# Optimization experiments

Measured on AMD Instinct MI355X. Metric: run time of the kernel, lower is better.

## Reference

```python
import math
import jax, jax.numpy as jnp
import numpy as np

# ---- model dims ----
D = 4096          # hidden_size
N = 32            # num_attention_heads (== num_key_value_heads)
Q_LORA = 1536
KV_LORA = 512
QK_NOPE = 128
QK_ROPE = 64
QK_HEAD = QK_NOPE + QK_ROPE   # 192
V_HEAD = 128
EPS = 1e-6
T = 2048

# ---- yarn rope constants ----
ROPE_THETA = 10000.0
FACTOR = 40.0
ORIG_MAX = 4096
BETA_FAST = 32.0
BETA_SLOW = 1.0
MSCALE = 1.0
MSCALE_ALL_DIM = 1.0


def _yarn_get_mscale(scale, mscale):
    if scale <= 1.0:
        return 1.0
    return 0.1 * mscale * math.log(scale) + 1.0

# softmax scale: qk_head_dim^-0.5 * yarn_mscale^2 (rope_mscale_all_dim = 1.0)
YARN_MSCALE = _yarn_get_mscale(FACTOR, MSCALE_ALL_DIM)
SM_SCALE = QK_HEAD ** (-0.5) * YARN_MSCALE ** 2


def _yarn_cos_sin(positions):
    """DeepSeek yarn scaled rotary embeddings. positions: int [T]."""
    half = QK_ROPE // 2
    pow_ = np.arange(0, QK_ROPE, 2, dtype=np.float64) / QK_ROPE
    pos_freqs = ROPE_THETA ** pow_
    inv_extra = 1.0 / pos_freqs
    inv_inter = 1.0 / (FACTOR * pos_freqs)

    def corr_dim(n_rot):
        return (QK_ROPE * math.log(ORIG_MAX / (n_rot * 2 * math.pi))) / (2 * math.log(ROPE_THETA))

    low = max(math.floor(corr_dim(BETA_FAST)), 0)
    high = min(math.ceil(corr_dim(BETA_SLOW)), QK_ROPE - 1)
    ramp = np.clip((np.arange(half, dtype=np.float64) - low) / max(high - low, 1e-3), 0.0, 1.0)
    mask = 1.0 - ramp  # 1 where extrapolation
    inv_freq = inv_inter * (1.0 - mask) + inv_extra * mask
    inv_freq = jnp.asarray(inv_freq, jnp.float32)

    mscale_coef = _yarn_get_mscale(FACTOR, MSCALE) / _yarn_get_mscale(FACTOR, MSCALE_ALL_DIM)
    t = positions.astype(jnp.float32)
    freqs = t[:, None] * inv_freq[None, :]          # [T, half]
    return jnp.cos(freqs) * mscale_coef, jnp.sin(freqs) * mscale_coef


def _apply_rope(x_tnh, cos, sin):
    """Neox-style (split halves) rope. x: [T, N, QK_ROPE]; cos/sin: [T, half]."""
    half = QK_ROPE // 2
    x1, x2 = x_tnh[..., :half], x_tnh[..., half:]
    c, s = cos[:, None, :], sin[:, None, :]
    return jnp.concatenate([x1 * c - x2 * s, x1 * s + x2 * c], axis=-1)


def _rms_norm(x, scale, eps=EPS):
    var = jnp.mean(jnp.square(x), axis=-1, keepdims=True)
    return x * jax.lax.rsqrt(var + eps) * scale


def setup_inputs() -> dict:
    key = jax.random.key(0)
    ks = jax.random.split(key, 8)
    std = 0.02
    return {
        "x": jax.random.normal(ks[0], (T, D), jnp.float32),
        "positions": jnp.arange(T, dtype=jnp.int32),
        "w_q_down": jax.random.normal(ks[1], (D, Q_LORA), jnp.float32) * std,
        "q_norm_scale": jnp.ones((Q_LORA,), jnp.float32),
        "w_q_up": jax.random.normal(ks[2], (Q_LORA, N, QK_HEAD), jnp.float32) * std,
        "w_kv_down": jax.random.normal(ks[3], (D, KV_LORA + QK_ROPE), jnp.float32) * std,
        "kv_norm_scale": jnp.ones((KV_LORA,), jnp.float32),
        "w_kv_up": jax.random.normal(ks[4], (KV_LORA, N, QK_NOPE + V_HEAD), jnp.float32) * std,
        "w_o": jax.random.normal(ks[5], (N, V_HEAD, D), jnp.float32) * std,
    }


def reference(x, positions, w_q_down, q_norm_scale, w_q_up, w_kv_down,
              kv_norm_scale, w_kv_up, w_o):
    cos, sin = _yarn_cos_sin(positions)

    # ---- q projection (low rank) ----
    q_ta = _rms_norm(jnp.einsum('td,da->ta', x, w_q_down), q_norm_scale)
    q_tnh = jnp.einsum('ta,anh->tnh', q_ta, w_q_up)            # [T,N,192]
    q_rope = _apply_rope(q_tnh[..., QK_NOPE:], cos, sin)
    q_tnh = jnp.concatenate([q_tnh[..., :QK_NOPE], q_rope], axis=-1)

    # ---- kv projection (compressed latent) ----
    kv_sa = jnp.einsum('sd,da->sa', x, w_kv_down)              # [T, KV_LORA+64]
    k_rope = _apply_rope(kv_sa[:, None, KV_LORA:], cos, sin)   # [T,1,64]
    k_rope = jnp.broadcast_to(k_rope, (x.shape[0], N, QK_ROPE))
    kv_lat = _rms_norm(kv_sa[..., :KV_LORA], kv_norm_scale)
    kv_nope = jnp.einsum('sa,anh->snh', kv_lat, w_kv_up)       # [T,N,256]
    k_snh = jnp.concatenate([kv_nope[..., :QK_NOPE], k_rope], axis=-1)
    v_snh = kv_nope[..., QK_NOPE:]

    # ---- causal attention (prefill; padding to 128-multiple is a no-op) ----
    scores = jnp.einsum('tnh,snh->nts', q_tnh, k_snh) * SM_SCALE
    tpos = jnp.arange(x.shape[0])
    causal = tpos[:, None] >= tpos[None, :]
    scores = jnp.where(causal[None, :, :], scores, jnp.finfo(scores.dtype).min)
    probs = jax.nn.softmax(scores, axis=-1)
    out_tnh = jnp.einsum('nts,snh->tnh', probs, v_snh)

    # ---- output projection ----
    return jnp.einsum('tnh,nhd->td', out_tnh, w_o)
```

## Files before the change

### kernel.cpp

```cpp
#include <hip/hip_runtime.h>
#include <math.h>
#include <stdint.h>

#define T_    2048
#define D_    4096
#define NH_   32
#define QL_   1536
#define KVL_  512
#define ROPE_ 64
#define NOPE_ 128
#define HQK_  192
#define HV_   128
#define KVD_  576
#define NCAT_ 2112

typedef __bf16 bf16x8 __attribute__((ext_vector_type(8)));
typedef __bf16 bf16x4 __attribute__((ext_vector_type(4)));
typedef float f32x4 __attribute__((ext_vector_type(4)));

__device__ __forceinline__ void gload_lds16(const __bf16* g, __bf16* l) {
  __builtin_amdgcn_global_load_lds(
      (const __attribute__((address_space(1))) void*)g,
      (__attribute__((address_space(3))) void*)l, 16, 0, 0);
}

template <typename OutT>
__global__ __launch_bounds__(256, 3) void mfma_gemm_kernel(
    const __bf16* __restrict__ A, const __bf16* __restrict__ Bt,
    OutT* __restrict__ C, int M, int Ncols, int K) {
  __shared__ __bf16 As[128 * 64];
  __shared__ __bf16 Bs[128 * 64];
  const int tid = threadIdx.x;
  const int lane = tid & 63;
  const int w = tid >> 6;
  const int wm = w >> 1, wn = w & 1;
  const int lg = lane >> 4, lj = lane & 15;
  const int bm = blockIdx.y * 128;
  const int bn = blockIdx.x * 128;

  const __bf16* ga[4]; const __bf16* gb[4];
  int ldsoff[4];
  #pragma unroll
  for (int i = 0; i < 4; ++i) {
    int task = i * 256 + tid;
    int r = task >> 3, cl = task & 7;
    int cg = cl ^ (r & 7);
    ga[i] = A  + (size_t)(bm + r) * K + cg * 8;
    gb[i] = Bt + (size_t)(bn + r) * K + cg * 8;
    ldsoff[i] = (i * 256 + w * 64) * 8;
  }

  f32x4 acc[4][4];
  #pragma unroll
  for (int mi = 0; mi < 4; ++mi)
    #pragma unroll
    for (int ni = 0; ni < 4; ++ni) acc[mi][ni] = (f32x4){0.f, 0.f, 0.f, 0.f};

  for (int k0 = 0; k0 < K; k0 += 64) {
    __syncthreads();
    #pragma unroll
    for (int i = 0; i < 4; ++i) gload_lds16(ga[i] + k0, &As[ldsoff[i]]);
    #pragma unroll
    for (int i = 0; i < 4; ++i) gload_lds16(gb[i] + k0, &Bs[ldsoff[i]]);
    __syncthreads();
    #pragma unroll
    for (int kh = 0; kh < 2; ++kh) {
      bf16x8 af[4], bfr[4];
      #pragma unroll
      for (int i = 0; i < 4; ++i) {
        int ra = wm * 64 + i * 16 + lj;
        af[i] = *(const bf16x8*)&As[ra * 64 + ((((kh << 2) + lg) ^ (ra & 7)) << 3)];
      }
      #pragma unroll
      for (int i = 0; i < 4; ++i) {
        int rb = wn * 64 + i * 16 + lj;
        bfr[i] = *(const bf16x8*)&Bs[rb * 64 + ((((kh << 2) + lg) ^ (rb & 7)) << 3)];
      }
      #pragma unroll
      for (int mi = 0; mi < 4; ++mi)
        #pragma unroll
        for (int ni = 0; ni < 4; ++ni)
          acc[mi][ni] = __builtin_amdgcn_mfma_f32_16x16x32_bf16(af[mi], bfr[ni], acc[mi][ni], 0, 0, 0);
    }
  }

  #pragma unroll
  for (int mi = 0; mi < 4; ++mi) {
    #pragma unroll
    for (int r = 0; r < 4; ++r) {
      int row = bm + wm * 64 + mi * 16 + lg * 4 + r;
      #pragma unroll
      for (int ni = 0; ni < 4; ++ni) {
        int col = bn + wn * 64 + ni * 16 + lj;
        if (col < Ncols) C[(size_t)row * Ncols + col] = (OutT)acc[mi][ni][r];
      }
    }
  }
}

__global__ __launch_bounds__(256) void transpose_bf16_kernel(
    const float* __restrict__ B, __bf16* __restrict__ Bt, int K, int N) {
  __shared__ float tile[64][65];
  int n0 = blockIdx.x * 64, k0 = blockIdx.y * 64;
  int tid = threadIdx.x;
  int kr = tid >> 4, nc = (tid & 15) * 4;
  #pragma unroll
  for (int i = 0; i < 4; ++i) {
    int k = kr + i * 16;
    float4 v = make_float4(0.f, 0.f, 0.f, 0.f);
    if (n0 + nc < N) v = *(const float4*)(B + (size_t)(k0 + k) * N + n0 + nc);
    tile[k][nc + 0] = v.x; tile[k][nc + 1] = v.y;
    tile[k][nc + 2] = v.z; tile[k][nc + 3] = v.w;
  }
  __syncthreads();
  int nl = tid >> 4, k4 = (tid & 15) * 4;
  #pragma unroll
  for (int i = 0; i < 4; ++i) {
    int nn = nl + i * 16;
    bf16x4 o;
    o[0] = (__bf16)tile[k4 + 0][nn]; o[1] = (__bf16)tile[k4 + 1][nn];
    o[2] = (__bf16)tile[k4 + 2][nn]; o[3] = (__bf16)tile[k4 + 3][nn];
    *(bf16x4*)(Bt + (size_t)(n0 + nn) * K + k0 + k4) = o;
  }
}

__global__ __launch_bounds__(256) void conv_bf16_kernel(
    const float* __restrict__ in, __bf16* __restrict__ out, int n8) {
  int i = blockIdx.x * 256 + threadIdx.x;
  if (i >= n8) return;
  float4 a = *(const float4*)(in + (size_t)i * 8);
  float4 b = *(const float4*)(in + (size_t)i * 8 + 4);
  bf16x8 v;
  v[0] = (__bf16)a.x; v[1] = (__bf16)a.y; v[2] = (__bf16)a.z; v[3] = (__bf16)a.w;
  v[4] = (__bf16)b.x; v[5] = (__bf16)b.y; v[6] = (__bf16)b.z; v[7] = (__bf16)b.w;
  *(bf16x8*)(out + (size_t)i * 8) = v;
}

__global__ __launch_bounds__(256) void rmsnorm_bf16_kernel(
    const float* __restrict__ in, __bf16* __restrict__ out,
    const float* __restrict__ scale, int len, int in_stride) {
  int row = blockIdx.x;
  const float* x = in + (size_t)row * in_stride;
  __bf16* y = out + (size_t)row * len;
  float ss = 0.f;
  for (int i = threadIdx.x; i < len; i += 256) { float v = x[i]; ss += v * v; }
  __shared__ float red[4];
  #pragma unroll
  for (int o = 32; o > 0; o >>= 1) ss += __shfl_down(ss, o, 64);
  int wid = threadIdx.x >> 6, lane = threadIdx.x & 63;
  if (lane == 0) red[wid] = ss;
  __syncthreads();
  if (threadIdx.x == 0) {
    float t = red[0] + red[1] + red[2] + red[3];
    red[0] = 1.0f / sqrtf(t / (float)len + 1e-6f);
  }
  __syncthreads();
  float r = red[0];
  for (int i = threadIdx.x; i < len; i += 256) y[i] = (__bf16)(x[i] * r * scale[i]);
}

struct InvFreq { float f[32]; };
__global__ __launch_bounds__(256) void rope_table_kernel(
    const int* __restrict__ pos, float* __restrict__ cosT, float* __restrict__ sinT,
    InvFreq invf) {
  int idx = blockIdx.x * 256 + threadIdx.x;
  if (idx >= T_ * 32) return;
  int t = idx >> 5, i = idx & 31;
  float fr = (float)pos[t] * invf.f[i];
  cosT[idx] = cosf(fr);
  sinT[idx] = sinf(fr);
}

__global__ __launch_bounds__(256) void rope_q_kernel(
    __bf16* __restrict__ q, const float* __restrict__ cosT, const float* __restrict__ sinT) {
  int idx = blockIdx.x * 256 + threadIdx.x;
  if (idx >= T_ * NH_ * 32) return;
  int i = idx & 31;
  int tn = idx >> 5;
  int t = tn >> 5;
  __bf16* b = q + (size_t)tn * HQK_ + NOPE_;
  float x1 = (float)b[i], x2 = (float)b[i + 32];
  float c = cosT[t * 32 + i], s = sinT[t * 32 + i];
  b[i]      = (__bf16)(x1 * c - x2 * s);
  b[i + 32] = (__bf16)(x1 * s + x2 * c);
}

__global__ __launch_bounds__(256) void rope_k_kernel(
    const float* __restrict__ src, int stride, const float* __restrict__ cosT,
    const float* __restrict__ sinT, __bf16* __restrict__ k_rope) {
  int idx = blockIdx.x * 256 + threadIdx.x;
  if (idx >= T_ * 32) return;
  int t = idx >> 5, i = idx & 31;
  const float* b = src + (size_t)t * stride;
  float x1 = b[i], x2 = b[i + 32];
  float c = cosT[idx], s = sinT[idx];
  k_rope[t * 64 + i]      = (__bf16)(x1 * c - x2 * s);
  k_rope[t * 64 + i + 32] = (__bf16)(x1 * s + x2 * c);
}

__global__ __launch_bounds__(256) void prep_vt_kernel(
    const __bf16* __restrict__ kv_nopeb, __bf16* __restrict__ Vt) {
  __shared__ __bf16 tile[64][136];
  int s0 = blockIdx.x * 64;
  int n = blockIdx.y;
  int tid = threadIdx.x;
  #pragma unroll
  for (int i = 0; i < 4; ++i) {
    int idx = tid + i * 256;
    int s = idx >> 4, c = idx & 15;
    bf16x8 v = *(const bf16x8*)(kv_nopeb + ((size_t)(s0 + s) * NH_ + n) * 256 + NOPE_ + c * 8);
    *(bf16x8*)&tile[s][c * 8] = v;
  }
  __syncthreads();
  #pragma unroll
  for (int i = 0; i < 8; ++i) {
    int idx = tid + i * 256;
    int h = idx >> 4, s4 = (idx & 15) * 4;
    bf16x4 v;
    v[0] = tile[s4 + 0][h]; v[1] = tile[s4 + 1][h];
    v[2] = tile[s4 + 2][h]; v[3] = tile[s4 + 3][h];
    *(bf16x4*)(Vt + ((size_t)n * HV_ + h) * T_ + s0 + s4) = v;
  }
}

__global__ __launch_bounds__(256) void attn_mfma_kernel(
    const __bf16* __restrict__ q_tnh, const __bf16* __restrict__ kv_nopeb,
    const __bf16* __restrict__ k_rope, const __bf16* __restrict__ Vt,
    __bf16* __restrict__ attn_out, float sm_scale2) {
  __shared__ __bf16 KsL[2][24 * 64 * 8];
  __shared__ __bf16 Vs[8 * 128 * 8];
  __shared__ __bf16 Ps[4][16 * 64];
  const int tid = threadIdx.x;
  const int lane = tid & 63;
  const int w = tid >> 6;
  const int id = blockIdx.x;
  const int j = id >> 3;
  const int qt = 31 - (j >> 2);
  const int n = (id & 7) * 4 + (j & 3);
  const int t0 = qt * 64;
  const int lg = lane >> 4;
  const int lj = lane & 15;
  const int rowbase = t0 + w * 16;

  const __bf16* kptr[6]; size_t kstep[6]; int klds[6];
  #pragma unroll
  for (int i = 0; i < 6; ++i) {
    int task = i * 256 + tid;
    int c = task >> 6, s = task & 63;
    if (c < 16) { kptr[i] = kv_nopeb + ((size_t)s * NH_ + n) * 256 + c * 8; kstep[i] = (size_t)64 * NH_ * 256; }
    else        { kptr[i] = k_rope + (size_t)s * ROPE_ + (c - 16) * 8;      kstep[i] = (size_t)64 * ROPE_; }
    klds[i] = (i * 256 + w * 64) * 8;
  }
  const __bf16* vptr[4]; int vlds[4];
  #pragma unroll
  for (int i = 0; i < 4; ++i) {
    int task = i * 256 + tid;
    int c = task >> 7, h = task & 127;
    vptr[i] = Vt + ((size_t)n * HV_ + h) * T_ + c * 8;
    vlds[i] = (i * 256 + w * 64) * 8;
  }

  #define STAGE_K(bufIdx)                                                      \
    do {                                                                       \
      __bf16* kb_ = &KsL[bufIdx][0];                                           \
      _Pragma("unroll")                                                        \
      for (int i_ = 0; i_ < 6; ++i_) {                                         \
        gload_lds16(kptr[i_], kb_ + klds[i_]);                                 \
        kptr[i_] += kstep[i_];                                                 \
      }                                                                        \
    } while (0)
  #define STAGE_V()                                                            \
    do {                                                                       \
      _Pragma("unroll")                                                        \
      for (int i_ = 0; i_ < 4; ++i_) {                                         \
        gload_lds16(vptr[i_], &Vs[0] + vlds[i_]);                              \
        vptr[i_] += 64;                                                        \
      }                                                                        \
    } while (0)

  STAGE_K(0);

  bf16x8 qf[6];
  {
    int t = t0 + w * 16 + lj;
    const __bf16* qp = q_tnh + ((size_t)t * NH_ + n) * HQK_;
    #pragma unroll
    for (int kk = 0; kk < 6; ++kk) {
      bf16x8 raw = *(const bf16x8*)(qp + kk * 32 + lg * 8);
      bf16x8 v;
      #pragma unroll
      for (int i = 0; i < 8; ++i) v[i] = (__bf16)((float)raw[i] * sm_scale2);
      qf[kk] = v;
    }
  }

  f32x4 O[8];
  #pragma unroll
  for (int nb = 0; nb < 8; ++nb) O[nb] = (f32x4){0.f, 0.f, 0.f, 0.f};
  float m_r[4], l_r[4];
  #pragma unroll
  for (int r = 0; r < 4; ++r) { m_r[r] = -1e30f; l_r[r] = 0.f; }

  __syncthreads();

  const int nst = qt + 1;
  #pragma unroll 1
  for (int st = 0; st < nst; ++st) {
    const int s0 = st * 64;
    const int cur = st & 1;
    if (st + 1 < nst) STAGE_K(cur ^ 1);
    STAGE_V();
    const __bf16* kb = &KsL[cur][0];

    f32x4 S[4];
    __builtin_amdgcn_s_setprio(1);
    #pragma unroll
    for (int sb = 0; sb < 4; ++sb) {
      f32x4 acc = (f32x4){0.f, 0.f, 0.f, 0.f};
      int srow = sb * 16 + lj;
      #pragma unroll
      for (int kk = 0; kk < 6; ++kk) {
        int c = kk * 4 + lg;
        bf16x8 b = *(const bf16x8*)&kb[(c * 64 + srow) * 8];
        acc = __builtin_amdgcn_mfma_f32_16x16x32_bf16(qf[kk], b, acc, 0, 0, 0);
      }
      S[sb] = acc;
    }
    __builtin_amdgcn_s_setprio(0);
    if (st == qt) {
      #pragma unroll
      for (int sb = 0; sb < 4; ++sb)
        #pragma unroll
        for (int r = 0; r < 4; ++r) {
          int row = rowbase + lg * 4 + r;
          int col = s0 + sb * 16 + lj;
          if (col > row) S[sb][r] = -1e30f;
        }
    }
    float mx[4];
    #pragma unroll
    for (int r = 0; r < 4; ++r) {
      float m2 = fmaxf(fmaxf(S[0][r], S[1][r]), fmaxf(S[2][r], S[3][r]));
      m2 = fmaxf(m2, __shfl_xor(m2, 1));
      m2 = fmaxf(m2, __shfl_xor(m2, 2));
      m2 = fmaxf(m2, __shfl_xor(m2, 4));
      m2 = fmaxf(m2, __shfl_xor(m2, 8));
      mx[r] = m2;
    }
    int need = (mx[0] > m_r[0]) | (mx[1] > m_r[1]) | (mx[2] > m_r[2]) | (mx[3] > m_r[3]);
    if (__any(need)) {
      #pragma unroll
      for (int r = 0; r < 4; ++r) {
        float mnew = fmaxf(m_r[r], mx[r]);
        float corr = __builtin_amdgcn_exp2f(m_r[r] - mnew);
        m_r[r] = mnew;
        l_r[r] *= corr;
        #pragma unroll
        for (int nb = 0; nb < 8; ++nb) O[nb][r] = O[nb][r] * corr;
      }
    }
    #pragma unroll
    for (int r = 0; r < 4; ++r) {
      float psum = 0.f;
      #pragma unroll
      for (int sb = 0; sb < 4; ++sb) {
        float pp = __builtin_amdgcn_exp2f(S[sb][r] - m_r[r]);
        S[sb][r] = pp;
        psum += pp;
      }
      l_r[r] += psum;
    }
    #pragma unroll
    for (int sb = 0; sb < 4; ++sb) {
      int sl = sb * 16 + lj;
      int c = sl >> 3;
      #pragma unroll
      for (int r = 0; r < 4; ++r) {
        int rw = lg * 4 + r;
        Ps[w][rw * 64 + ((c ^ (rw & 7)) << 3) + (sl & 7)] = (__bf16)S[sb][r];
      }
    }
    __syncthreads();
    __builtin_amdgcn_s_setprio(1);
    #pragma unroll
    for (int kk = 0; kk < 2; ++kk) {
      int ca = kk * 4 + lg;
      bf16x8 pa = *(const bf16x8*)&Ps[w][lj * 64 + ((ca ^ (lj & 7)) << 3)];
      #pragma unroll
      for (int nb = 0; nb < 8; ++nb) {
        int h = nb * 16 + lj;
        bf16x8 bv = *(const bf16x8*)&Vs[(ca * 128 + h) * 8];
        O[nb] = __builtin_amdgcn_mfma_f32_16x16x32_bf16(pa, bv, O[nb], 0, 0, 0);
      }
    }
    __builtin_amdgcn_s_setprio(0);
    __syncthreads();
  }

  #pragma unroll
  for (int r = 0; r < 4; ++r) {
    float lsum = l_r[r];
    lsum += __shfl_xor(lsum, 1);
    lsum += __shfl_xor(lsum, 2);
    lsum += __shfl_xor(lsum, 4);
    lsum += __shfl_xor(lsum, 8);
    float inv = 1.0f / lsum;
    int t = t0 + w * 16 + lg * 4 + r;
    __bf16* dst = attn_out + ((size_t)t * NH_ + n) * HV_;
    #pragma unroll
    for (int nb = 0; nb < 8; ++nb) dst[nb * 16 + lj] = (__bf16)(O[nb][r] * inv);
  }
  #undef STAGE_K
  #undef STAGE_V
}

static void compute_inv_freq(float* out) {
  const double theta = 10000.0, factor = 40.0;
  const double PI = 3.14159265358979323846;
  const int rot = ROPE_;
  double low_d  = rot * log(4096.0 / (32.0 * 2.0 * PI)) / (2.0 * log(theta));
  double high_d = rot * log(4096.0 / ( 1.0 * 2.0 * PI)) / (2.0 * log(theta));
  double low = floor(low_d);  if (low < 0) low = 0;
  double high = ceil(high_d); if (high > rot - 1) high = rot - 1;
  for (int i = 0; i < 32; ++i) {
    double pf = pow(theta, (2.0 * i) / (double)rot);
    double inv_extra = 1.0 / pf;
    double inv_inter = 1.0 / (factor * pf);
    double ramp = ((double)i - low) / fmax(high - low, 0.001);
    ramp = fmin(fmax(ramp, 0.0), 1.0);
    double mask = 1.0 - ramp;
    out[i] = (float)(inv_inter * (1.0 - mask) + inv_extra * mask);
  }
}

extern "C" void kernel_launch(void* const* d_in, const int* in_sizes, int n_in,
                              void* d_out, int out_size, void* d_ws, size_t ws_size,
                              hipStream_t stream) {
  const float* x            = (const float*)d_in[0];
  const int*   positions    = (const int*)d_in[1];
  const float* w_q_down     = (const float*)d_in[2];
  const float* q_norm_scale = (const float*)d_in[3];
  const float* w_q_up       = (const float*)d_in[4];
  const float* w_kv_down    = (const float*)d_in[5];
  const float* kv_norm_scale= (const float*)d_in[6];
  const float* w_kv_up      = (const float*)d_in[7];
  const float* w_o          = (const float*)d_in[8];
  float* out = (float*)d_out;

  float* ws = (float*)d_ws;
  float*  cosT     = ws;
  float*  sinT     = ws + 65536;
  float*  cat      = ws + 131072;
  __bf16* xb       = (__bf16*)(ws + 4456448);
  __bf16* Bt_cat   = (__bf16*)(ws + 8650752);
  __bf16* Bt_qu    = (__bf16*)(ws + 13107200);
  __bf16* Bt_kvu   = (__bf16*)(ws + 17825792);
  __bf16* q_tab    = (__bf16*)(ws + 19922944);
  __bf16* kv_latb  = (__bf16*)(ws + 21495808);
  __bf16* k_ropeb  = (__bf16*)(ws + 22020096);
  __bf16* q_tnhb   = (__bf16*)(ws + 22085632);
  __bf16* kv_nopeb = (__bf16*)(ws + 28377088);
  __bf16* Vt       = (__bf16*)(ws + 13107200);
  __bf16* attn_ob  = (__bf16*)(ws + 17825792);
  __bf16* Bt_o     = (__bf16*)(ws + 4456448);
  (void)ws_size; (void)n_in; (void)in_sizes; (void)out_size;

  InvFreq invf;
  compute_inv_freq(invf.f);
  double ym = 0.1 * log(40.0) + 1.0;
  float sm_scale2 = (float)((ym * ym / sqrt((double)HQK_)) * 1.44269504088896340736);

  rope_table_kernel<<<(T_ * 32 + 255) / 256, 256, 0, stream>>>(positions, cosT, sinT, invf);
  conv_bf16_kernel<<<T_ * D_ / 8 / 256, 256, 0, stream>>>(x, xb, T_ * D_ / 8);
  transpose_bf16_kernel<<<dim3(QL_ / 64, D_ / 64), 256, 0, stream>>>(w_q_down, Bt_cat, D_, QL_);
  transpose_bf16_kernel<<<dim3(KVD_ / 64, D_ / 64), 256, 0, stream>>>(w_kv_down, Bt_cat + (size_t)QL_ * D_, D_, KVD_);
  transpose_bf16_kernel<<<dim3(NH_ * HQK_ / 64, QL_ / 64), 256, 0, stream>>>(w_q_up, Bt_qu, QL_, NH_ * HQK_);
  transpose_bf16_kernel<<<dim3(NH_ * 256 / 64, KVL_ / 64), 256, 0, stream>>>(w_kv_up, Bt_kvu, KVL_, NH_ * 256);

  mfma_gemm_kernel<float><<<dim3((NCAT_ + 127) / 128, T_ / 128), 256, 0, stream>>>(xb, Bt_cat, cat, T_, NCAT_, D_);

  rmsnorm_bf16_kernel<<<T_, 256, 0, stream>>>(cat, q_tab, q_norm_scale, QL_, NCAT_);
  mfma_gemm_kernel<__bf16><<<dim3(NH_ * HQK_ / 128, T_ / 128), 256, 0, stream>>>(q_tab, Bt_qu, q_tnhb, T_, NH_ * HQK_, QL_);
  rope_q_kernel<<<(T_ * NH_ * 32 + 255) / 256, 256, 0, stream>>>(q_tnhb, cosT, sinT);

  rmsnorm_bf16_kernel<<<T_, 256, 0, stream>>>(cat + QL_, kv_latb, kv_norm_scale, KVL_, NCAT_);
  rope_k_kernel<<<(T_ * 32 + 255) / 256, 256, 0, stream>>>(cat + QL_ + KVL_, NCAT_, cosT, sinT, k_ropeb);
  mfma_gemm_kernel<__bf16><<<dim3(NH_ * 256 / 128, T_ / 128), 256, 0, stream>>>(kv_latb, Bt_kvu, kv_nopeb, T_, NH_ * 256, KVL_);

  prep_vt_kernel<<<dim3(T_ / 64, NH_), 256, 0, stream>>>(kv_nopeb, Vt);
  attn_mfma_kernel<<<1024, 256, 0, stream>>>(q_tnhb, kv_nopeb, k_ropeb, Vt, attn_ob, sm_scale2);

  transpose_bf16_kernel<<<dim3(D_ / 64, NH_ * HV_ / 64), 256, 0, stream>>>(w_o, Bt_o, NH_ * HV_, D_);
  mfma_gemm_kernel<float><<<dim3(D_ / 128, T_ / 128), 256, 0, stream>>>(attn_ob, Bt_o, out, T_, D_, NH_ * HV_);
}
```

Baseline: 422.7 us.

## Pair causal q-tiles per attention block to balance work and share K/V loads

Each attention block now processes two query tiles (p and 31-p) for the same head, so every block does the same number of KV steps, and the K/V tiles staged in LDS are reused for both. The grid is halved to 512 blocks, and launch bounds request two blocks per CU. The cost is doubled accumulator and Q-fragment registers plus a larger P buffer in LDS, which may limit occupancy or cause spills.

```diff
diff --git a/kernel.cpp b/kernel.cpp
--- a/kernel.cpp
+++ b/kernel.cpp
@@ -223,24 +223,23 @@
   }
 }
 
-__global__ __launch_bounds__(256) void attn_mfma_kernel(
+__global__ __launch_bounds__(256, 2) void attn_mfma_kernel(
     const __bf16* __restrict__ q_tnh, const __bf16* __restrict__ kv_nopeb,
     const __bf16* __restrict__ k_rope, const __bf16* __restrict__ Vt,
     __bf16* __restrict__ attn_out, float sm_scale2) {
   __shared__ __bf16 KsL[2][24 * 64 * 8];
   __shared__ __bf16 Vs[8 * 128 * 8];
-  __shared__ __bf16 Ps[4][16 * 64];
+  __shared__ __bf16 Ps[4][32 * 64];
   const int tid = threadIdx.x;
   const int lane = tid & 63;
   const int w = tid >> 6;
   const int id = blockIdx.x;
   const int j = id >> 3;
-  const int qt = 31 - (j >> 2);
+  const int p = j >> 2;
   const int n = (id & 7) * 4 + (j & 3);
-  const int t0 = qt * 64;
   const int lg = lane >> 4;
   const int lj = lane & 15;
-  const int rowbase = t0 + w * 16;
+  const int qtf0 = p, qtf1 = 31 - p;
 
   const __bf16* kptr[6]; size_t kstep[6]; int klds[6];
   #pragma unroll
@@ -280,9 +279,10 @@
 
   STAGE_K(0);
 
-  bf16x8 qf[6];
-  {
-    int t = t0 + w * 16 + lj;
+  bf16x8 qf[2][6];
+  #pragma unroll
+  for (int f = 0; f < 2; ++f) {
+    int t = (f ? qtf1 : qtf0) * 64 + w * 16 + lj;
     const __bf16* qp = q_tnh + ((size_t)t * NH_ + n) * HQK_;
     #pragma unroll
     for (int kk = 0; kk < 6; ++kk) {
@@ -290,20 +290,23 @@
       bf16x8 v;
       #pragma unroll
       for (int i = 0; i < 8; ++i) v[i] = (__bf16)((float)raw[i] * sm_scale2);
-      qf[kk] = v;
+      qf[f][kk] = v;
     }
   }
 
-  f32x4 O[8];
-  #pragma unroll
-  for (int nb = 0; nb < 8; ++nb) O[nb] = (f32x4){0.f, 0.f, 0.f, 0.f};
-  float m_r[4], l_r[4];
-  #pragma unroll
-  for (int r = 0; r < 4; ++r) { m_r[r] = -1e30f; l_r[r] = 0.f; }
+  f32x4 O[2][8];
+  float m_r[2][4], l_r[2][4];
+  #pragma unroll
+  for (int f = 0; f < 2; ++f) {
+    #pragma unroll
+    for (int nb = 0; nb < 8; ++nb) O[f][nb] = (f32x4){0.f, 0.f, 0.f, 0.f};
+    #pragma unroll
+    for (int r = 0; r < 4; ++r) { m_r[f][r] = -1e30f; l_r[f][r] = 0.f; }
+  }
 
   __syncthreads();
 
-  const int nst = qt + 1;
+  const int nst = 32 - p;
   #pragma unroll 1
   for (int st = 0; st < nst; ++st) {
     const int s0 = st * 64;
@@ -311,86 +314,98 @@
     if (st + 1 < nst) STAGE_K(cur ^ 1);
     STAGE_V();
     const __bf16* kb = &KsL[cur][0];
-
-    f32x4 S[4];
-    __builtin_amdgcn_s_setprio(1);
-    #pragma unroll
-    for (int sb = 0; sb < 4; ++sb) {
-      f32x4 acc = (f32x4){0.f, 0.f, 0.f, 0.f};
-      int srow = sb * 16 + lj;
-      #pragma unroll
-      for (int kk = 0; kk < 6; ++kk) {
-        int c = kk * 4 + lg;
-        bf16x8 b = *(const bf16x8*)&kb[(c * 64 + srow) * 8];
-        acc = __builtin_amdgcn_mfma_f32_16x16x32_bf16(qf[kk], b, acc, 0, 0, 0);
-      }
-      S[sb] = acc;
-    }
-    __builtin_amdgcn_s_setprio(0);
-    if (st == qt) {
-      #pragma unroll
-      for (int sb = 0; sb < 4; ++sb)
+    const bool act0 = (st <= qtf0);
+
+    #pragma unroll
+    for (int f = 0; f < 2; ++f) {
+      if (f == 0 && !act0) continue;
+      const int qt = f ? qtf1 : qtf0;
+      const int rowbase = qt * 64 + w * 16;
+      f32x4 S[4];
+      __builtin_amdgcn_s_setprio(1);
+      #pragma unroll
+      for (int sb = 0; sb < 4; ++sb) {
+        f32x4 acc = (f32x4){0.f, 0.f, 0.f, 0.f};
+        int srow = sb * 16 + lj;
+        #pragma unroll
+        for (int kk = 0; kk < 6; ++kk) {
+          int c = kk * 4 + lg;
+          bf16x8 b = *(const bf16x8*)&kb[(c * 64 + srow) * 8];
+          acc = __builtin_amdgcn_mfma_f32_16x16x32_bf16(qf[f][kk], b, acc, 0, 0, 0);
+        }
+        S[sb] = acc;
+      }
+      __builtin_amdgcn_s_setprio(0);
+      if (st == qt) {
+        #pragma unroll
+        for (int sb = 0; sb < 4; ++sb)
+          #pragma unroll
+          for (int r = 0; r < 4; ++r) {
+            int row = rowbase + lg * 4 + r;
+            int col = s0 + sb * 16 + lj;
+            if (col > row) S[sb][r] = -1e30f;
+          }
+      }
+      float mx[4];
+      #pragma unroll
+      for (int r = 0; r < 4; ++r) {
+        float m2 = fmaxf(fmaxf(S[0][r], S[1][r]), fmaxf(S[2][r], S[3][r]));
+        m2 = fmaxf(m2, __shfl_xor(m2, 1));
+        m2 = fmaxf(m2, __shfl_xor(m2, 2));
+        m2 = fmaxf(m2, __shfl_xor(m2, 4));
+        m2 = fmaxf(m2, __shfl_xor(m2, 8));
+        mx[r] = m2;
+      }
+      int need = (mx[0] > m_r[f][0]) | (mx[1] > m_r[f][1]) |
+                 (mx[2] > m_r[f][2]) | (mx[3] > m_r[f][3]);
+      if (__any(need)) {
         #pragma unroll
         for (int r = 0; r < 4; ++r) {
-          int row = rowbase + lg * 4 + r;
-          int col = s0 + sb * 16 + lj;
-          if (col > row) S[sb][r] = -1e30f;
+          float mnew = fmaxf(m_r[f][r], mx[r]);
+          float corr = __builtin_amdgcn_exp2f(m_r[f][r] - mnew);
+          m_r[f][r] = mnew;
+          l_r[f][r] *= corr;
+          #pragma unroll
+          for (int nb = 0; nb < 8; ++nb) O[f][nb][r] = O[f][nb][r] * corr;
         }
-    }
-    float mx[4];
-    #pragma unroll
-    for (int r = 0; r < 4; ++r) {
-      float m2 = fmaxf(fmaxf(S[0][r], S[1][r]), fmaxf(S[2][r], S[3][r]));
-      m2 = fmaxf(m2, __shfl_xor(m2, 1));
-      m2 = fmaxf(m2, __shfl_xor(m2, 2));
-      m2 = fmaxf(m2, __shfl_xor(m2, 4));
-      m2 = fmaxf(m2, __shfl_xor(m2, 8));
-      mx[r] = m2;
-    }
-    int need = (mx[0] > m_r[0]) | (mx[1] > m_r[1]) | (mx[2] > m_r[2]) | (mx[3] > m_r[3]);
-    if (__any(need)) {
+      }
       #pragma unroll
       for (int r = 0; r < 4; ++r) {
-        float mnew = fmaxf(m_r[r], mx[r]);
-        float corr = __builtin_amdgcn_exp2f(m_r[r] - mnew);
-        m_r[r] = mnew;
-        l_r[r] *= corr;
-        #pragma unroll
-        for (int nb = 0; nb < 8; ++nb) O[nb][r] = O[nb][r] * corr;
-      }
-    }
-    #pragma unroll
-    for (int r = 0; r < 4; ++r) {
-      float psum = 0.f;
+        float psum = 0.f;
+        #pragma unroll
+        for (int sb = 0; sb < 4; ++sb) {
+          float pp = __builtin_amdgcn_exp2f(S[sb][r] - m_r[f][r]);
+          S[sb][r] = pp;
+          psum += pp;
+        }
+        l_r[f][r] += psum;
+      }
       #pragma unroll
       for (int sb = 0; sb < 4; ++sb) {
-        float pp = __builtin_amdgcn_exp2f(S[sb][r] - m_r[r]);
-        S[sb][r] = pp;
-        psum += pp;
-      }
-      l_r[r] += psum;
-    }
-    #pragma unroll
-    for (int sb = 0; sb < 4; ++sb) {
-      int sl = sb * 16 + lj;
-      int c = sl >> 3;
-      #pragma unroll
-      for (int r = 0; r < 4; ++r) {
-        int rw = lg * 4 + r;
-        Ps[w][rw * 64 + ((c ^ (rw & 7)) << 3) + (sl & 7)] = (__bf16)S[sb][r];
+        int sl = sb * 16 + lj;
+        int c = sl >> 3;
+        #pragma unroll
+        for (int r = 0; r < 4; ++r) {
+          int rw = lg * 4 + r;
+          Ps[w][(f * 16 + rw) * 64 + ((c ^ (rw & 7)) << 3) + (sl & 7)] = (__bf16)S[sb][r];
+        }
       }
     }
     __syncthreads();
     __builtin_amdgcn_s_setprio(1);
     #pragma unroll
-    for (int kk = 0; kk < 2; ++kk) {
-      int ca = kk * 4 + lg;
-      bf16x8 pa = *(const bf16x8*)&Ps[w][lj * 64 + ((ca ^ (lj & 7)) << 3)];
-      #pragma unroll
-      for (int nb = 0; nb < 8; ++nb) {
-        int h = nb * 16 + lj;
-        bf16x8 bv = *(const bf16x8*)&Vs[(ca * 128 + h) * 8];
-        O[nb] = __builtin_amdgcn_mfma_f32_16x16x32_bf16(pa, bv, O[nb], 0, 0, 0);
+    for (int f = 0; f < 2; ++f) {
+      if (f == 0 && !act0) continue;
+      #pragma unroll
+      for (int kk = 0; kk < 2; ++kk) {
+        int ca = kk * 4 + lg;
+        bf16x8 pa = *(const bf16x8*)&Ps[w][(f * 16 + lj) * 64 + ((ca ^ (lj & 7)) << 3)];
+        #pragma unroll
+        for (int nb = 0; nb < 8; ++nb) {
+          int h = nb * 16 + lj;
+          bf16x8 bv = *(const bf16x8*)&Vs[(ca * 128 + h) * 8];
+          O[f][nb] = __builtin_amdgcn_mfma_f32_16x16x32_bf16(pa, bv, O[f][nb], 0, 0, 0);
+        }
       }
     }
     __builtin_amdgcn_s_setprio(0);
@@ -398,17 +413,21 @@
   }
 
   #pragma unroll
-  for (int r = 0; r < 4; ++r) {
-    float lsum = l_r[r];
-    lsum += __shfl_xor(lsum, 1);
-    lsum += __shfl_xor(lsum, 2);
-    lsum += __shfl_xor(lsum, 4);
-    lsum += __shfl_xor(lsum, 8);
-    float inv = 1.0f / lsum;
-    int t = t0 + w * 16 + lg * 4 + r;
-    __bf16* dst = attn_out + ((size_t)t * NH_ + n) * HV_;
-    #pragma unroll
-    for (int nb = 0; nb < 8; ++nb) dst[nb * 16 + lj] = (__bf16)(O[nb][r] * inv);
+  for (int f = 0; f < 2; ++f) {
+    const int qt = f ? qtf1 : qtf0;
+    #pragma unroll
+    for (int r = 0; r < 4; ++r) {
+      float lsum = l_r[f][r];
+      lsum += __shfl_xor(lsum, 1);
+      lsum += __shfl_xor(lsum, 2);
+      lsum += __shfl_xor(lsum, 4);
+      lsum += __shfl_xor(lsum, 8);
+      float inv = 1.0f / lsum;
+      int t = qt * 64 + w * 16 + lg * 4 + r;
+      __bf16* dst = attn_out + ((size_t)t * NH_ + n) * HV_;
+      #pragma unroll
+      for (int nb = 0; nb < 8; ++nb) dst[nb * 16 + lj] = (__bf16)(O[f][nb][r] * inv);
+    }
   }
   #undef STAGE_K
   #undef STAGE_V
@@ -488,7 +507,7 @@
   mfma_gemm_kernel<__bf16><<<dim3(NH_ * 256 / 128, T_ / 128), 256, 0, stream>>>(kv_latb, Bt_kvu, kv_nopeb, T_, NH_ * 256, KVL_);
 
   prep_vt_kernel<<<dim3(T_ / 64, NH_), 256, 0, stream>>>(kv_nopeb, Vt);
-  attn_mfma_kernel<<<1024, 256, 0, stream>>>(q_tnhb, kv_nopeb, k_ropeb, Vt, attn_ob, sm_scale2);
+  attn_mfma_kernel<<<512, 256, 0, stream>>>(q_tnhb, kv_nopeb, k_ropeb, Vt, attn_ob, sm_scale2);
 
   transpose_bf16_kernel<<<dim3(D_ / 64, NH_ * HV_ / 64), 256, 0, stream>>>(w_o, Bt_o, NH_ * HV_, D_);
   mfma_gemm_kernel<float><<<dim3(D_ / 128, T_ / 128), 256, 0, stream>>>(attn_ob, Bt_o, out, T_, D_, NH_ * HV_);
```

Measured after the change: 413.9 us. 1.02x faster.
